# Kernel tuning notes

Measured on AMD Instinct MI355X. Metric: run time of the kernel, lower is better.

## Reference

```python
import jax, jax.numpy as jnp
import numpy as np
from jax import lax

T, B = 16, 8192

def _linear_init(key, out_f, in_f):
    bound = 1.0 / np.sqrt(in_f)
    kw, kb = jax.random.split(key)
    W = jax.random.uniform(kw, (out_f, in_f), jnp.float32, -bound, bound)
    b = jax.random.uniform(kb, (out_f,), jnp.float32, -bound, bound)
    return W, b

def setup_inputs() -> dict:
    key = jax.random.key(0)
    ks = jax.random.split(key, 10)
    x = jax.random.normal(ks[0], (T, B, 64), jnp.float32)
    cue = jax.random.normal(ks[1], (T, B, 2), jnp.float32)
    hc1 = jax.random.normal(ks[2], (B, 256), jnp.float32)
    hc2 = jax.random.normal(ks[3], (B, 256), jnp.float32)
    hc3 = jax.random.normal(ks[4], (B, 256), jnp.float32)
    hc4 = jax.random.normal(ks[5], (B, 256), jnp.float32)
    W_i2h, b_i2h = _linear_init(ks[6], 256, 64)
    W_h2h, b_h2h = _linear_init(ks[7], 256, 256)
    W_h2o, b_h2o = _linear_init(ks[8], 64, 256)
    W_fcc, b_fcc = _linear_init(ks[9], 8, 64)
    return dict(x=x, cue=cue, hc1=hc1, hc2=hc2, hc3=hc3, hc4=hc4,
                W_i2h=W_i2h, b_i2h=b_i2h, W_h2h=W_h2h, b_h2h=b_h2h,
                W_h2o=W_h2o, b_h2o=b_h2o, W_fcc=W_fcc, b_fcc=b_fcc)

def reference(x, cue, hc1, hc2, hc3, hc4,
              W_i2h, b_i2h, W_h2h, b_h2h, W_h2o, b_h2o, W_fcc, b_fcc):
    # Input projection has no cross-step dependency: batch it over all 16 steps.
    i2h_seq = jnp.einsum('tbi,hi->tbh', x, W_i2h) + b_i2h  # [T,B,256]

    def step(h, i2h_t):
        h2h = h @ W_h2h.T + b_h2h          # [B,256]
        h_new = jnp.tanh(i2h_t + h2h)      # Elman recurrence
        return h_new, (h_new, h2h)

    hc1_final, (hs, h2h_seq) = lax.scan(step, hc1, i2h_seq)
    # Output head is also batchable over time.
    out = jnp.tanh(jnp.einsum('tbh,oh->tbo', hs, W_h2o) + b_h2o)  # [T,B,64]
    output_seq = jnp.einsum('tbo,co->tbc', out, W_fcc) + b_fcc    # [T,B,8]
    # Original also returns several torch.empty (uninitialized) buffers and the
    # untouched hc2..hc4; we return the meaningful computed tensors + pass-throughs.
    return (output_seq, hc1_final, hc2, hc3, hc4, i2h_seq, h2h_seq)
```

## Files before the change

### kernel.cpp

```cpp
#include <hip/hip_runtime.h>

typedef __bf16 bf16_t;
typedef bf16_t bf16x8 __attribute__((ext_vector_type(8)));
typedef float floatx4 __attribute__((ext_vector_type(4)));
typedef unsigned short ushort_t;

#define HLD 264
#define OLD 68

__device__ __forceinline__ floatx4 mfma16(bf16x8 a, bf16x8 b, floatx4 c) {
  return __builtin_amdgcn_mfma_f32_16x16x32_bf16(a, b, c, 0, 0, 0);
}

__device__ __forceinline__ float tanh_fast(float x) {
  x = fminf(15.0f, fmaxf(-15.0f, x));
  float e = __expf(-2.0f * x);
  return (1.0f - e) / (1.0f + e);
}

__device__ __forceinline__ bf16x8 cvt8(floatx4 f0, floatx4 f1) {
  bf16x8 r;
  r[0] = (bf16_t)f0[0]; r[1] = (bf16_t)f0[1]; r[2] = (bf16_t)f0[2]; r[3] = (bf16_t)f0[3];
  r[4] = (bf16_t)f1[0]; r[5] = (bf16_t)f1[1]; r[6] = (bf16_t)f1[2]; r[7] = (bf16_t)f1[3];
  return r;
}

__global__ void pack_all(const float* __restrict__ Wh2h, const float* __restrict__ Wi2h,
                         const float* __restrict__ Wh2o, ushort_t* __restrict__ ws) {
  int id = blockIdx.x * 256 + threadIdx.x;
  const float* W; int ldk, ksteps; ushort_t* dst; int rel;
  if (id < 8192)       { W = Wh2h; ldk = 256; ksteps = 8; dst = ws;         rel = id; }
  else if (id < 10240) { W = Wi2h; ldk = 64;  ksteps = 2; dst = ws + 65536; rel = id - 8192; }
  else if (id < 12288) { W = Wh2o; ldk = 256; ksteps = 8; dst = ws + 81920; rel = id - 10240; }
  else return;
  int lane = rel & 63, fi = rel >> 6;
  int kstep = fi % ksteps, ntile = fi / ksteps;
  int n  = ntile * 16 + (lane & 15);
  int k0 = kstep * 32 + ((lane >> 4) << 3);
  const float* src = W + (size_t)n * ldk + k0;
  floatx4 f0 = *(const floatx4*)src;
  floatx4 f1 = *(const floatx4*)(src + 4);
  ((bf16x8*)dst)[rel] = cvt8(f0, f1);
}

__global__ __launch_bounds__(512, 2)
void rnn_fused(const float* __restrict__ x,
               const float* __restrict__ hc1,
               const float* __restrict__ hc2,
               const float* __restrict__ hc3,
               const float* __restrict__ hc4,
               const float* __restrict__ b_i2h,
               const float* __restrict__ b_h2h,
               const float* __restrict__ b_h2o,
               const float* __restrict__ W_fcc,
               const float* __restrict__ b_fcc,
               const ushort_t* __restrict__ wsW,
               float* __restrict__ out_seq,
               float* __restrict__ hc1_f,
               float* __restrict__ hc2_o,
               float* __restrict__ hc3_o,
               float* __restrict__ hc4_o,
               float* __restrict__ i2h_seq,
               float* __restrict__ h2h_seq) {
  __shared__ bf16_t h_lds[32 * HLD];
  __shared__ float  out_s[32 * OLD];
  __shared__ float  wfcc_s[8 * OLD];

  const int tid  = threadIdx.x;
  const int lane = tid & 63;
  const int wv   = tid >> 6;
  const int q    = lane >> 4;
  const int c    = lane & 15;
  const int r0   = blockIdx.x * 32;

  const bf16x8* WH = (const bf16x8*)(wsW);
  const bf16x8* WI = (const bf16x8*)(wsW + 65536);
  const bf16x8* WO = (const bf16x8*)(wsW + 81920);

  {
    const floatx4* s2 = (const floatx4*)(hc2 + (size_t)r0 * 256);
    const floatx4* s3 = (const floatx4*)(hc3 + (size_t)r0 * 256);
    const floatx4* s4 = (const floatx4*)(hc4 + (size_t)r0 * 256);
    floatx4* d2 = (floatx4*)(hc2_o + (size_t)r0 * 256);
    floatx4* d3 = (floatx4*)(hc3_o + (size_t)r0 * 256);
    floatx4* d4 = (floatx4*)(hc4_o + (size_t)r0 * 256);
    for (int i = tid; i < 2048; i += 512) { d2[i] = s2[i]; d3[i] = s3[i]; d4[i] = s4[i]; }
  }

  for (int i = tid; i < 2048; i += 512) {
    int m = i >> 6, k4 = (i & 63) * 4;
    floatx4 v = *(const floatx4*)&hc1[(size_t)(r0 + m) * 256 + k4];
    h_lds[m * HLD + k4 + 0] = (bf16_t)v[0];
    h_lds[m * HLD + k4 + 1] = (bf16_t)v[1];
    h_lds[m * HLD + k4 + 2] = (bf16_t)v[2];
    h_lds[m * HLD + k4 + 3] = (bf16_t)v[3];
  }
  {
    int o = tid >> 6, i = tid & 63;
    if (tid < 512) wfcc_s[o * OLD + i] = W_fcc[tid];
  }

  const int n0 = wv * 2;
  const float bI0 = b_i2h[n0 * 16 + c], bI1 = b_i2h[(n0 + 1) * 16 + c];
  const float bH0 = b_h2h[n0 * 16 + c], bH1 = b_h2h[(n0 + 1) * 16 + c];
  const int mo = wv >> 2, no = wv & 3;
  const float bO = b_h2o[no * 16 + c];
  const int fm = tid >> 3, fo = tid & 7;
  const float bF = b_fcc[fo];

  bf16x8 wh[8][2], wi[2][2], wo[8];
#pragma unroll
  for (int k = 0; k < 8; ++k) {
    wh[k][0] = WH[((n0)     * 8 + k) * 64 + lane];
    wh[k][1] = WH[((n0 + 1) * 8 + k) * 64 + lane];
    wo[k]    = WO[(no * 8 + k) * 64 + lane];
  }
#pragma unroll
  for (int k = 0; k < 2; ++k) {
    wi[k][0] = WI[((n0)     * 2 + k) * 64 + lane];
    wi[k][1] = WI[((n0 + 1) * 2 + k) * 64 + lane];
  }

  __syncthreads();

  for (int t = 0; t < 16; ++t) {
    floatx4 accH[2][2], accI[2][2];
#pragma unroll
    for (int a = 0; a < 2; ++a)
#pragma unroll
      for (int b = 0; b < 2; ++b) { accH[a][b] = (floatx4){0,0,0,0}; accI[a][b] = (floatx4){0,0,0,0}; }

#pragma unroll
    for (int k = 0; k < 8; ++k) {
      bf16x8 a0 = *(const bf16x8*)&h_lds[(c)      * HLD + k * 32 + q * 8];
      bf16x8 a1 = *(const bf16x8*)&h_lds[(16 + c) * HLD + k * 32 + q * 8];
      accH[0][0] = mfma16(a0, wh[k][0], accH[0][0]);
      accH[1][0] = mfma16(a1, wh[k][0], accH[1][0]);
      accH[0][1] = mfma16(a0, wh[k][1], accH[0][1]);
      accH[1][1] = mfma16(a1, wh[k][1], accH[1][1]);
    }
    const float* xt = x + ((size_t)t * 8192 + r0) * 64;
#pragma unroll
    for (int k = 0; k < 2; ++k) {
      const float* p0 = xt + (c)      * 64 + k * 32 + q * 8;
      const float* p1 = xt + (16 + c) * 64 + k * 32 + q * 8;
      bf16x8 a0 = cvt8(*(const floatx4*)p0, *(const floatx4*)(p0 + 4));
      bf16x8 a1 = cvt8(*(const floatx4*)p1, *(const floatx4*)(p1 + 4));
      accI[0][0] = mfma16(a0, wi[k][0], accI[0][0]);
      accI[1][0] = mfma16(a1, wi[k][0], accI[1][0]);
      accI[0][1] = mfma16(a0, wi[k][1], accI[0][1]);
      accI[1][1] = mfma16(a1, wi[k][1], accI[1][1]);
    }

    float hnew[2][2][4];
    const size_t bt = (size_t)t * 8192 + r0;
#pragma unroll
    for (int mt = 0; mt < 2; ++mt) {
#pragma unroll
      for (int nl = 0; nl < 2; ++nl) {
        const float bIv = nl ? bI1 : bI0;
        const float bHv = nl ? bH1 : bH0;
#pragma unroll
        for (int rg = 0; rg < 4; ++rg) {
          int row = mt * 16 + q * 4 + rg;
          int col = (n0 + nl) * 16 + c;
          size_t gi = (bt + row) * 256 + col;
          float vi = accI[mt][nl][rg] + bIv;
          float vh = accH[mt][nl][rg] + bHv;
          i2h_seq[gi] = vi;
          h2h_seq[gi] = vh;
          float hv = tanh_fast(vi + vh);
          hnew[mt][nl][rg] = hv;
          if (t == 15) hc1_f[(size_t)(r0 + row) * 256 + col] = hv;
        }
      }
    }
    __syncthreads();
#pragma unroll
    for (int mt = 0; mt < 2; ++mt)
#pragma unroll
      for (int nl = 0; nl < 2; ++nl)
#pragma unroll
        for (int rg = 0; rg < 4; ++rg)
          h_lds[(mt * 16 + q * 4 + rg) * HLD + (n0 + nl) * 16 + c] = (bf16_t)hnew[mt][nl][rg];
    __syncthreads();

    floatx4 accO = (floatx4){0,0,0,0};
#pragma unroll
    for (int k = 0; k < 8; ++k) {
      bf16x8 a = *(const bf16x8*)&h_lds[(mo * 16 + c) * HLD + k * 32 + q * 8];
      accO = mfma16(a, wo[k], accO);
    }
#pragma unroll
    for (int rg = 0; rg < 4; ++rg)
      out_s[(mo * 16 + q * 4 + rg) * OLD + no * 16 + c] = tanh_fast(accO[rg] + bO);
    __syncthreads();

    if (tid < 256) {
      float s = bF;
#pragma unroll
      for (int i4 = 0; i4 < 16; ++i4) {
        floatx4 a = *(const floatx4*)&out_s[fm * OLD + i4 * 4];
        floatx4 w = *(const floatx4*)&wfcc_s[fo * OLD + i4 * 4];
        s += a[0]*w[0] + a[1]*w[1] + a[2]*w[2] + a[3]*w[3];
      }
      out_seq[(bt + fm) * 8 + fo] = s;
    }
  }
}

extern "C" void kernel_launch(void* const* d_in, const int* in_sizes, int n_in,
                              void* d_out, int out_size, void* d_ws, size_t ws_size,
                              hipStream_t stream) {
  (void)in_sizes; (void)n_in; (void)out_size; (void)ws_size;
  const float* x     = (const float*)d_in[0];
  const float* hc1   = (const float*)d_in[2];
  const float* hc2   = (const float*)d_in[3];
  const float* hc3   = (const float*)d_in[4];
  const float* hc4   = (const float*)d_in[5];
  const float* W_i2h = (const float*)d_in[6];
  const float* b_i2h = (const float*)d_in[7];
  const float* W_h2h = (const float*)d_in[8];
  const float* b_h2h = (const float*)d_in[9];
  const float* W_h2o = (const float*)d_in[10];
  const float* b_h2o = (const float*)d_in[11];
  const float* W_fcc = (const float*)d_in[12];
  const float* b_fcc = (const float*)d_in[13];

  float* out     = (float*)d_out;
  float* out_seq = out;
  float* hc1_f   = out + 1048576;
  float* hc2_o   = out + 3145728;
  float* hc3_o   = out + 5242880;
  float* hc4_o   = out + 7340032;
  float* i2h_seq = out + 9437184;
  float* h2h_seq = out + 42991616;

  ushort_t* ws = (ushort_t*)d_ws;

  pack_all<<<48, 256, 0, stream>>>(W_h2h, W_i2h, W_h2o, ws);
  rnn_fused<<<256, 512, 0, stream>>>(x, hc1, hc2, hc3, hc4,
                                     b_i2h, b_h2h, b_h2o, W_fcc, b_fcc,
                                     (const ushort_t*)ws,
                                     out_seq, hc1_f, hc2_o, hc3_o, hc4_o,
                                     i2h_seq, h2h_seq);
}
```

Measured before the change: 402.2 us.

## Double-buffer hidden state and output tiles to cut per-step barriers

Double-buffers the hidden-state tile and the output scratch in LDS, so each time step needs a single __syncthreads instead of three. The final fc projection is deferred by one step, with an epilogue that handles the last step. The step's x loads are also issued before the recurrent MFMAs, the i2h/h2h stores become nontemporal, and the hc2..hc4 pass-through copies are spread across the time loop. This is meant to cut barrier stalls and hide global memory latency, at the cost of more LDS and more complex ordering.

```diff
diff --git a/kernel.cpp b/kernel.cpp
--- a/kernel.cpp
+++ b/kernel.cpp
@@ -62,8 +62,8 @@
                float* __restrict__ hc4_o,
                float* __restrict__ i2h_seq,
                float* __restrict__ h2h_seq) {
-  __shared__ bf16_t h_lds[32 * HLD];
-  __shared__ float  out_s[32 * OLD];
+  __shared__ bf16_t h_lds[2][32 * HLD];
+  __shared__ float  out_s[2][32 * OLD];
   __shared__ float  wfcc_s[8 * OLD];
 
   const int tid  = threadIdx.x;
@@ -77,28 +77,15 @@
   const bf16x8* WI = (const bf16x8*)(wsW + 65536);
   const bf16x8* WO = (const bf16x8*)(wsW + 81920);
 
-  {
-    const floatx4* s2 = (const floatx4*)(hc2 + (size_t)r0 * 256);
-    const floatx4* s3 = (const floatx4*)(hc3 + (size_t)r0 * 256);
-    const floatx4* s4 = (const floatx4*)(hc4 + (size_t)r0 * 256);
-    floatx4* d2 = (floatx4*)(hc2_o + (size_t)r0 * 256);
-    floatx4* d3 = (floatx4*)(hc3_o + (size_t)r0 * 256);
-    floatx4* d4 = (floatx4*)(hc4_o + (size_t)r0 * 256);
-    for (int i = tid; i < 2048; i += 512) { d2[i] = s2[i]; d3[i] = s3[i]; d4[i] = s4[i]; }
-  }
-
   for (int i = tid; i < 2048; i += 512) {
     int m = i >> 6, k4 = (i & 63) * 4;
     floatx4 v = *(const floatx4*)&hc1[(size_t)(r0 + m) * 256 + k4];
-    h_lds[m * HLD + k4 + 0] = (bf16_t)v[0];
-    h_lds[m * HLD + k4 + 1] = (bf16_t)v[1];
-    h_lds[m * HLD + k4 + 2] = (bf16_t)v[2];
-    h_lds[m * HLD + k4 + 3] = (bf16_t)v[3];
-  }
-  {
-    int o = tid >> 6, i = tid & 63;
-    if (tid < 512) wfcc_s[o * OLD + i] = W_fcc[tid];
-  }
+    h_lds[0][m * HLD + k4 + 0] = (bf16_t)v[0];
+    h_lds[0][m * HLD + k4 + 1] = (bf16_t)v[1];
+    h_lds[0][m * HLD + k4 + 2] = (bf16_t)v[2];
+    h_lds[0][m * HLD + k4 + 3] = (bf16_t)v[3];
+  }
+  { int o = tid >> 6, i = tid & 63; if (tid < 512) wfcc_s[o * OLD + i] = W_fcc[tid]; }
 
   const int n0 = wv * 2;
   const float bI0 = b_i2h[n0 * 16 + c], bI1 = b_i2h[(n0 + 1) * 16 + c];
@@ -124,6 +111,19 @@
   __syncthreads();
 
   for (int t = 0; t < 16; ++t) {
+    const int p = t & 1;
+    const size_t bt = (size_t)t * 8192 + r0;
+
+    const float* xt = x + bt * 64;
+    floatx4 xv[2][4];
+#pragma unroll
+    for (int k = 0; k < 2; ++k) {
+      const float* p0 = xt + (c)      * 64 + k * 32 + q * 8;
+      const float* p1 = xt + (16 + c) * 64 + k * 32 + q * 8;
+      xv[k][0] = *(const floatx4*)p0;  xv[k][1] = *(const floatx4*)(p0 + 4);
+      xv[k][2] = *(const floatx4*)p1;  xv[k][3] = *(const floatx4*)(p1 + 4);
+    }
+
     floatx4 accH[2][2], accI[2][2];
 #pragma unroll
     for (int a = 0; a < 2; ++a)
@@ -132,80 +132,95 @@
 
 #pragma unroll
     for (int k = 0; k < 8; ++k) {
-      bf16x8 a0 = *(const bf16x8*)&h_lds[(c)      * HLD + k * 32 + q * 8];
-      bf16x8 a1 = *(const bf16x8*)&h_lds[(16 + c) * HLD + k * 32 + q * 8];
+      bf16x8 a0 = *(const bf16x8*)&h_lds[p][(c)      * HLD + k * 32 + q * 8];
+      bf16x8 a1 = *(const bf16x8*)&h_lds[p][(16 + c) * HLD + k * 32 + q * 8];
       accH[0][0] = mfma16(a0, wh[k][0], accH[0][0]);
       accH[1][0] = mfma16(a1, wh[k][0], accH[1][0]);
       accH[0][1] = mfma16(a0, wh[k][1], accH[0][1]);
       accH[1][1] = mfma16(a1, wh[k][1], accH[1][1]);
     }
-    const float* xt = x + ((size_t)t * 8192 + r0) * 64;
 #pragma unroll
     for (int k = 0; k < 2; ++k) {
-      const float* p0 = xt + (c)      * 64 + k * 32 + q * 8;
-      const float* p1 = xt + (16 + c) * 64 + k * 32 + q * 8;
-      bf16x8 a0 = cvt8(*(const floatx4*)p0, *(const floatx4*)(p0 + 4));
-      bf16x8 a1 = cvt8(*(const floatx4*)p1, *(const floatx4*)(p1 + 4));
+      bf16x8 a0 = cvt8(xv[k][0], xv[k][1]);
+      bf16x8 a1 = cvt8(xv[k][2], xv[k][3]);
       accI[0][0] = mfma16(a0, wi[k][0], accI[0][0]);
       accI[1][0] = mfma16(a1, wi[k][0], accI[1][0]);
       accI[0][1] = mfma16(a0, wi[k][1], accI[0][1]);
       accI[1][1] = mfma16(a1, wi[k][1], accI[1][1]);
     }
 
-    float hnew[2][2][4];
-    const size_t bt = (size_t)t * 8192 + r0;
-#pragma unroll
-    for (int mt = 0; mt < 2; ++mt) {
+#pragma unroll
+    for (int mt = 0; mt < 2; ++mt)
 #pragma unroll
       for (int nl = 0; nl < 2; ++nl) {
         const float bIv = nl ? bI1 : bI0;
         const float bHv = nl ? bH1 : bH0;
+#pragma unroll
+        for (int rg = 0; rg < 4; ++rg) {
+          accI[mt][nl][rg] += bIv;
+          accH[mt][nl][rg] += bHv;
+          float hv = tanh_fast(accI[mt][nl][rg] + accH[mt][nl][rg]);
+          h_lds[1 - p][(mt * 16 + q * 4 + rg) * HLD + (n0 + nl) * 16 + c] = (bf16_t)hv;
+        }
+      }
+
+    __syncthreads();
+
+#pragma unroll
+    for (int mt = 0; mt < 2; ++mt)
+#pragma unroll
+      for (int nl = 0; nl < 2; ++nl)
 #pragma unroll
         for (int rg = 0; rg < 4; ++rg) {
           int row = mt * 16 + q * 4 + rg;
           int col = (n0 + nl) * 16 + c;
           size_t gi = (bt + row) * 256 + col;
-          float vi = accI[mt][nl][rg] + bIv;
-          float vh = accH[mt][nl][rg] + bHv;
-          i2h_seq[gi] = vi;
-          h2h_seq[gi] = vh;
-          float hv = tanh_fast(vi + vh);
-          hnew[mt][nl][rg] = hv;
-          if (t == 15) hc1_f[(size_t)(r0 + row) * 256 + col] = hv;
+          __builtin_nontemporal_store(accI[mt][nl][rg], &i2h_seq[gi]);
+          __builtin_nontemporal_store(accH[mt][nl][rg], &h2h_seq[gi]);
+          if (t == 15)
+            hc1_f[(size_t)(r0 + row) * 256 + col] =
+                tanh_fast(accI[mt][nl][rg] + accH[mt][nl][rg]);
         }
-      }
-    }
-    __syncthreads();
-#pragma unroll
-    for (int mt = 0; mt < 2; ++mt)
-#pragma unroll
-      for (int nl = 0; nl < 2; ++nl)
-#pragma unroll
-        for (int rg = 0; rg < 4; ++rg)
-          h_lds[(mt * 16 + q * 4 + rg) * HLD + (n0 + nl) * 16 + c] = (bf16_t)hnew[mt][nl][rg];
-    __syncthreads();
-
-    floatx4 accO = (floatx4){0,0,0,0};
-#pragma unroll
-    for (int k = 0; k < 8; ++k) {
-      bf16x8 a = *(const bf16x8*)&h_lds[(mo * 16 + c) * HLD + k * 32 + q * 8];
-      accO = mfma16(a, wo[k], accO);
-    }
-#pragma unroll
-    for (int rg = 0; rg < 4; ++rg)
-      out_s[(mo * 16 + q * 4 + rg) * OLD + no * 16 + c] = tanh_fast(accO[rg] + bO);
-    __syncthreads();
-
-    if (tid < 256) {
+
+    if (tid < 384) {
+      int tensor = tid >> 7, j = (tid & 127) + t * 128;
+      const float* s = tensor == 0 ? hc2 : (tensor == 1 ? hc3 : hc4);
+      float*       d = tensor == 0 ? hc2_o : (tensor == 1 ? hc3_o : hc4_o);
+      ((floatx4*)(d + (size_t)r0 * 256))[j] = ((const floatx4*)(s + (size_t)r0 * 256))[j];
+    }
+
+    if (t > 0 && tid < 256) {
       float s = bF;
 #pragma unroll
       for (int i4 = 0; i4 < 16; ++i4) {
-        floatx4 a = *(const floatx4*)&out_s[fm * OLD + i4 * 4];
+        floatx4 a = *(const floatx4*)&out_s[1 - p][fm * OLD + i4 * 4];
         floatx4 w = *(const floatx4*)&wfcc_s[fo * OLD + i4 * 4];
         s += a[0]*w[0] + a[1]*w[1] + a[2]*w[2] + a[3]*w[3];
       }
-      out_seq[(bt + fm) * 8 + fo] = s;
-    }
+      out_seq[((size_t)(t - 1) * 8192 + r0 + fm) * 8 + fo] = s;
+    }
+
+    floatx4 accO = (floatx4){0,0,0,0};
+#pragma unroll
+    for (int k = 0; k < 8; ++k) {
+      bf16x8 a = *(const bf16x8*)&h_lds[1 - p][(mo * 16 + c) * HLD + k * 32 + q * 8];
+      accO = mfma16(a, wo[k], accO);
+    }
+#pragma unroll
+    for (int rg = 0; rg < 4; ++rg)
+      out_s[p][(mo * 16 + q * 4 + rg) * OLD + no * 16 + c] = tanh_fast(accO[rg] + bO);
+  }
+
+  __syncthreads();
+  if (tid < 256) {
+    float s = bF;
+#pragma unroll
+    for (int i4 = 0; i4 < 16; ++i4) {
+      floatx4 a = *(const floatx4*)&out_s[1][fm * OLD + i4 * 4];
+      floatx4 w = *(const floatx4*)&wfcc_s[fo * OLD + i4 * 4];
+      s += a[0]*w[0] + a[1]*w[1] + a[2]*w[2] + a[3]*w[3];
+    }
+    out_seq[((size_t)15 * 8192 + r0 + fm) * 8 + fo] = s;
   }
 }
 
```

Measured after the change: 402.0 us. Within noise of the previous version (-0.1%).
